# Performance work log

Measured on AMD Instinct MI355X. Metric: run time of the kernel, lower is better.

The kernel has to match this reference:

```python
import jax, jax.numpy as jnp
import numpy as np

B, D, H, C = 8192, 2048, 4096, 64
HALF = D // 2
BLOCKS = 2


def setup_inputs() -> dict:
    key = jax.random.key(0)
    ks = jax.random.split(key, 8)
    z = jax.random.normal(ks[0], (B, D), jnp.float32)
    condition = jax.random.normal(ks[1], (B, C), jnp.float32)
    # alternating masks: block 0 identity=odd indices, transform=even; block 1 flipped
    even = jnp.arange(0, D, 2, dtype=jnp.int32)
    odd = jnp.arange(1, D, 2, dtype=jnp.int32)
    idx_id = jnp.stack([odd, even])   # [BLOCKS, HALF]
    idx_tr = jnp.stack([even, odd])   # [BLOCKS, HALF]
    def init_w(k, shape, fan_in):
        return jax.random.normal(k, shape, jnp.float32) * np.float32(1.0 / np.sqrt(fan_in))
    W1 = init_w(ks[2], (BLOCKS, HALF + C, H), HALF + C)
    b1 = jnp.zeros((BLOCKS, H), jnp.float32)
    W2 = init_w(ks[3], (BLOCKS, H, H), H)
    b2 = jnp.zeros((BLOCKS, H), jnp.float32)
    W3 = init_w(ks[4], (BLOCKS, H, 2 * HALF), H) * np.float32(0.01)  # keep exp(S) tame
    b3 = jnp.zeros((BLOCKS, 2 * HALF), jnp.float32)
    return {"z": z, "condition": condition, "idx_id": idx_id, "idx_tr": idx_tr,
            "W1": W1, "b1": b1, "W2": W2, "b2": b2, "W3": W3, "b3": b3}


def reference(z, condition, idx_id, idx_tr, W1, b1, W2, b2, W3, b3):
    # F_zx of the affine coupling layer (scale_tanh=False, clamp_scale=None)
    x = z
    log_det = jnp.zeros((z.shape[0], 1), z.dtype)
    for i in range(BLOCKS):
        # gather identity channels, condition on external vector
        h = jnp.concatenate([x[:, idx_id[i]], condition], axis=-1)  # [B, HALF+C]
        h = jax.nn.relu(h @ W1[i] + b1[i])
        h = jax.nn.relu(h @ W2[i] + b2[i])
        out = (h @ W3[i] + b3[i]).reshape(x.shape[0], HALF, 2)
        S = out[..., 0]  # scale logits
        T = out[..., 1]  # translation
        # scatter-update transformed channels
        x = x.at[:, idx_tr[i]].set(x[:, idx_tr[i]] * jnp.exp(S) + T)
        log_det = log_det + jnp.sum(S, axis=1, keepdims=True)
    return x, log_det
```

## Files before the change

### kernel.cpp

```cpp
#include <hip/hip_runtime.h>
#include <hip/hip_bf16.h>

#define B_    8192
#define D_    2048
#define H_    4096
#define C_    64
#define HALF_ 1024
#define KIN_  1088

typedef __attribute__((ext_vector_type(8))) short bf16x8;
typedef __attribute__((ext_vector_type(4))) float f32x4;

__device__ __forceinline__ unsigned short f2bf(float f) {
  __hip_bfloat16 h = __float2bfloat16(f);
  return *reinterpret_cast<unsigned short*>(&h);
}

__device__ __forceinline__ void gload16(const void* g, void* s) {
  __builtin_amdgcn_global_load_lds((const __attribute__((address_space(1))) void*)g,
                                   (__attribute__((address_space(3))) void*)s,
                                   16, 0, 0);
}

__global__ void convT(const float* __restrict__ W, unsigned short* __restrict__ Wt,
                      int K, int N) {
  __shared__ float tile[32][33];
  int tx = threadIdx.x & 31, ty = threadIdx.x >> 5;
  int n0 = blockIdx.x * 32, k0 = blockIdx.y * 32;
#pragma unroll
  for (int i = 0; i < 4; ++i)
    tile[ty + i * 8][tx] = W[(size_t)(k0 + ty + i * 8) * N + n0 + tx];
  __syncthreads();
#pragma unroll
  for (int i = 0; i < 4; ++i)
    Wt[(size_t)(n0 + ty + i * 8) * K + k0 + tx] = f2bf(tile[tx][ty + i * 8]);
}

__global__ void build_act(const float* __restrict__ xsrc, const float* __restrict__ cond,
                          int par, unsigned short* __restrict__ A0) {
  int row = blockIdx.y;
  int col = blockIdx.x * 256 + threadIdx.x;
  if (col >= KIN_) return;
  float v = (col < HALF_) ? xsrc[(size_t)row * D_ + col * 2 + par]
                          : cond[(size_t)row * C_ + (col - HALF_)];
  A0[(size_t)row * KIN_ + col] = f2bf(v);
}

template <int MODE>
__global__ __launch_bounds__(512, 2)
void gemm8p(const unsigned short* __restrict__ A,
            const unsigned short* __restrict__ Bt,
            const float* __restrict__ bias,
            unsigned short* __restrict__ Cout,
            const float* __restrict__ xold, float* __restrict__ xnew,
            float* __restrict__ part, int par,
            int M, int N, int K) {
  __shared__ unsigned short lds[65536];
  char* ldsb = (char*)lds;
  const int tid = threadIdx.x;
  const int w = tid >> 6, lane = tid & 63;
  const int fr = lane & 15, fq = lane >> 4;
  const int wr = w >> 2, wc = w & 3;

  const int nbx = N >> 8;
  const int nwg = (int)gridDim.x;
  const int cpx = nwg >> 3;
  const int bid = (int)blockIdx.x;
  const int swz = (bid & 7) * cpx + (bid >> 3);
  const int by = swz / nbx, bx = swz - by * nbx;
  const int m0 = by << 8, n0 = bx << 8;

  const int chunkp = (((fr & 1) << 2) | fq) ^ (fr >> 1);
  const int A0 = (wr * 64 + (fr >> 1)) * 128 + chunkp * 16;
  const int B0 = 32768 + (wc * 32 + (fr >> 1)) * 128 + chunkp * 16;

  int rS[2], kcolS[2];
#pragma unroll
  for (int s = 0; s < 2; ++s) {
    int q = s * 512 + w * 64 + lane;
    int p = q >> 3, cph = q & 7;
    int clg = cph ^ (p & 7);
    rS[s] = 2 * p + (clg >> 2);
    kcolS[s] = (clg & 3) * 8;
  }
  const unsigned short* sA0 = A + (size_t)(m0 + rS[0]) * K + kcolS[0];
  const unsigned short* sA1 = A + (size_t)(m0 + rS[1]) * K + kcolS[1];
  const unsigned short* sB0 = Bt + (size_t)(n0 + rS[0]) * K + kcolS[0];
  const unsigned short* sB1 = Bt + (size_t)(n0 + rS[1]) * K + kcolS[1];
  const int dst0 = w * 1024 + lane * 16;

#define STAGE_A(KK, TILE, BUF) do {                                          \
    gload16(sA0 + (TILE) * 64 + (KK) * 32,                                   \
            ldsb + (BUF) + (KK) * 16384 + dst0);                             \
    gload16(sA1 + (TILE) * 64 + (KK) * 32,                                   \
            ldsb + (BUF) + (KK) * 16384 + 8192 + dst0);                      \
  } while (0)
#define STAGE_B(KK, TILE, BUF) do {                                          \
    gload16(sB0 + (TILE) * 64 + (KK) * 32,                                   \
            ldsb + (BUF) + 32768 + (KK) * 16384 + dst0);                     \
    gload16(sB1 + (TILE) * 64 + (KK) * 32,                                   \
            ldsb + (BUF) + 32768 + (KK) * 16384 + 8192 + dst0);              \
  } while (0)

  f32x4 acc[8][4];
  f32x4 z4 = {0.f, 0.f, 0.f, 0.f};
#pragma unroll
  for (int m = 0; m < 8; ++m)
#pragma unroll
    for (int n = 0; n < 4; ++n) acc[m][n] = z4;

  const int NT = K >> 6;

  STAGE_A(0, 0, 0);
  STAGE_A(1, 0, 0);
  STAGE_B(0, 0, 0);
  STAGE_B(1, 0, 0);
  STAGE_B(0, 1, 65536);
  STAGE_A(0, 1, 65536);
  STAGE_B(1, 1, 65536);
  asm volatile("s_waitcnt vmcnt(6)" ::: "memory");
  __builtin_amdgcn_sched_barrier(0);
  __builtin_amdgcn_s_barrier();

#define PHASE_TAIL()                                                         \
    __builtin_amdgcn_sched_barrier(0);                                       \
    __builtin_amdgcn_s_barrier();                                            \
    asm volatile("s_waitcnt lgkmcnt(0)" ::: "memory");                       \
    __builtin_amdgcn_sched_barrier(0);

#define TILE8(TT, S1, S234, DO_VM)                                           \
  {                                                                          \
    const int bufC = ((TT) & 1) * 65536;                                     \
    const int bufN = 65536 - bufC;                                           \
    bf16x8 av[4], bv[4];                                                     \
                               \
    _Pragma("unroll") for (int m = 0; m < 4; ++m)                            \
      av[m] = *(const bf16x8*)(ldsb + bufC + A0 + m * 1024);                 \
    _Pragma("unroll") for (int n = 0; n < 4; ++n)                            \
      bv[n] = *(const bf16x8*)(ldsb + bufC + B0 + n * 1024);                 \
    if (S1) { STAGE_A(1, (TT) + 1, bufN); }                                  \
    PHASE_TAIL()                                                             \
    __builtin_amdgcn_s_setprio(1);                                           \
    _Pragma("unroll") for (int m = 0; m < 4; ++m)                            \
      _Pragma("unroll") for (int n = 0; n < 4; ++n)                          \
        acc[m][n] = __builtin_amdgcn_mfma_f32_16x16x32_bf16(av[m], bv[n],    \
                                                        acc[m][n], 0, 0, 0); \
    __builtin_amdgcn_s_setprio(0);                                           \
    __builtin_amdgcn_sched_barrier(0);                                       \
    __builtin_amdgcn_s_barrier();                                            \
                                 \
    _Pragma("unroll") for (int m = 0; m < 4; ++m)                            \
      av[m] = *(const bf16x8*)(ldsb + bufC + A0 + (m + 4) * 1024);           \
    if (S234) { STAGE_B(0, (TT) + 2, bufC); }                                \
    PHASE_TAIL()                                                             \
    __builtin_amdgcn_s_setprio(1);                                           \
    _Pragma("unroll") for (int m = 0; m < 4; ++m)                            \
      _Pragma("unroll") for (int n = 0; n < 4; ++n)                          \
        acc[m + 4][n] = __builtin_amdgcn_mfma_f32_16x16x32_bf16(av[m], bv[n],\
                                                    acc[m + 4][n], 0, 0, 0); \
    __builtin_amdgcn_s_setprio(0);                                           \
    __builtin_amdgcn_sched_barrier(0);                                       \
    __builtin_amdgcn_s_barrier();                                            \
                               \
    _Pragma("unroll") for (int m = 0; m < 4; ++m)                            \
      av[m] = *(const bf16x8*)(ldsb + bufC + A0 + m * 1024 + 16384);         \
    _Pragma("unroll") for (int n = 0; n < 4; ++n)                            \
      bv[n] = *(const bf16x8*)(ldsb + bufC + B0 + n * 1024 + 16384);         \
    if (S234) { STAGE_A(0, (TT) + 2, bufC); }                                \
    PHASE_TAIL()                                                             \
    __builtin_amdgcn_s_setprio(1);                                           \
    _Pragma("unroll") for (int m = 0; m < 4; ++m)                            \
      _Pragma("unroll") for (int n = 0; n < 4; ++n)                          \
        acc[m][n] = __builtin_amdgcn_mfma_f32_16x16x32_bf16(av[m], bv[n],    \
                                                        acc[m][n], 0, 0, 0); \
    __builtin_amdgcn_s_setprio(0);                                           \
    __builtin_amdgcn_sched_barrier(0);                                       \
    __builtin_amdgcn_s_barrier();                                            \
                                           \
    _Pragma("unroll") for (int m = 0; m < 4; ++m)                            \
      av[m] = *(const bf16x8*)(ldsb + bufC + A0 + (m + 4) * 1024 + 16384);   \
    if (S234) { STAGE_B(1, (TT) + 2, bufC); }                                \
    PHASE_TAIL()                                                             \
    __builtin_amdgcn_s_setprio(1);                                           \
    _Pragma("unroll") for (int m = 0; m < 4; ++m)                            \
      _Pragma("unroll") for (int n = 0; n < 4; ++n)                          \
        acc[m + 4][n] = __builtin_amdgcn_mfma_f32_16x16x32_bf16(av[m], bv[n],\
                                                    acc[m + 4][n], 0, 0, 0); \
    __builtin_amdgcn_s_setprio(0);                                           \
    __builtin_amdgcn_sched_barrier(0);                                       \
    if (DO_VM == 1) asm volatile("s_waitcnt vmcnt(6)" ::: "memory");         \
    if (DO_VM == 2) asm volatile("s_waitcnt vmcnt(0)" ::: "memory");         \
    __builtin_amdgcn_sched_barrier(0);                                       \
    __builtin_amdgcn_s_barrier();                                            \
  }

  for (int T = 0; T < NT - 2; ++T) {
    TILE8(T, 1, 1, 1)
  }
  TILE8(NT - 2, 1, 0, 2)
  TILE8(NT - 1, 0, 0, 0)
#undef TILE8
#undef PHASE_TAIL
#undef STAGE_A
#undef STAGE_B

  if (MODE == 0) {
#pragma unroll
    for (int m = 0; m < 8; ++m)
#pragma unroll
      for (int n = 0; n < 4; ++n) {
        int gcol = n0 + wc * 64 + n * 16 + fr;
        float bb = bias[gcol];
#pragma unroll
        for (int r = 0; r < 4; ++r) {
          float v = fmaxf(acc[m][n][r] + bb, 0.f);
          int lrow = m * 16 + fq * 4 + r;
          *(unsigned short*)(ldsb + w * 16384 + lrow * 128 + ((n ^ fq) * 32) + fr * 2) = f2bf(v);
        }
      }
    asm volatile("s_waitcnt lgkmcnt(0)" ::: "memory");
    __builtin_amdgcn_sched_barrier(0);
    unsigned short* Cb = Cout + (size_t)(m0 + wr * 128) * N + n0 + wc * 64;
    const int sub = lane & 7;
#pragma unroll
    for (int i = 0; i < 16; ++i) {
      int lrow = i * 8 + (lane >> 3);
      int phys = (sub >> 1) ^ ((lrow >> 2) & 3);
      bf16x8 val = *(const bf16x8*)(ldsb + w * 16384 + lrow * 128 + phys * 32 + (sub & 1) * 16);
      *(bf16x8*)(Cb + (size_t)lrow * N + sub * 8) = val;
    }
  } else {
#pragma unroll
    for (int m = 0; m < 8; ++m) {
      float srow[4] = {0.f, 0.f, 0.f, 0.f};
#pragma unroll
      for (int n = 0; n < 4; ++n) {
        int gcol = n0 + wc * 64 + n * 16 + fr;
        float bb = bias[gcol];
#pragma unroll
        for (int r = 0; r < 4; ++r) {
          float v = acc[m][n][r] + bb;
          float vp = __shfl_xor(v, 1);
          if (!(fr & 1)) {
            int grow = m0 + wr * 128 + m * 16 + fq * 4 + r;
            float xo = xold[(size_t)grow * N + gcol + par];
            xnew[(size_t)grow * N + gcol + par] = xo * expf(v) + vp;
            srow[r] += v;
          }
        }
      }
#pragma unroll
      for (int r = 0; r < 4; ++r) {
        float s = srow[r];
        s += __shfl_xor(s, 2);
        s += __shfl_xor(s, 4);
        s += __shfl_xor(s, 8);
        if (fr == 0) {
          int grow = m0 + wr * 128 + m * 16 + fq * 4 + r;
          part[(size_t)grow * 32 + bx * 4 + wc] = s;
        }
      }
    }
  }
}

__global__ void reduce_logdet(const float* __restrict__ P, float* __restrict__ logdet, int add) {
  int row = blockIdx.x * 256 + threadIdx.x;
  float s = 0.f;
#pragma unroll
  for (int g = 0; g < 32; ++g) s += P[(size_t)row * 32 + g];
  logdet[row] = add ? (logdet[row] + s) : s;
}

extern "C" void kernel_launch(void* const* d_in, const int* in_sizes, int n_in,
                              void* d_out, int out_size, void* d_ws, size_t ws_size,
                              hipStream_t stream) {
  const float* z    = (const float*)d_in[0];
  const float* cond = (const float*)d_in[1];
  const float* W1   = (const float*)d_in[4];
  const float* b1   = (const float*)d_in[5];
  const float* W2   = (const float*)d_in[6];
  const float* b2   = (const float*)d_in[7];
  const float* W3   = (const float*)d_in[8];
  const float* b3   = (const float*)d_in[9];

  float* xout   = (float*)d_out;
  float* logdet = xout + (size_t)B_ * D_;

  char* ws = (char*)d_ws;
  unsigned short* Wt = (unsigned short*)ws;
  unsigned short* H1 = (unsigned short*)(ws + 33554432);
  unsigned short* H2 = (unsigned short*)(ws + 33554432 + 67108864);
  float* Pp = (float*)H1;
  unsigned short* A0 = H2;

  for (int blk = 0; blk < 2; ++blk) {
    const float* W1b = W1 + (size_t)blk * KIN_ * H_;
    const float* W2b = W2 + (size_t)blk * H_ * H_;
    const float* W3b = W3 + (size_t)blk * H_ * D_;
    const float* b1b = b1 + (size_t)blk * H_;
    const float* b2b = b2 + (size_t)blk * H_;
    const float* b3b = b3 + (size_t)blk * D_;
    const float* xsrc = blk ? xout : z;

    convT<<<dim3(H_ / 32, KIN_ / 32), 256, 0, stream>>>(W1b, Wt, KIN_, H_);
    build_act<<<dim3(5, B_), 256, 0, stream>>>(xsrc, cond, 1 - blk, A0);
    gemm8p<0><<<dim3((H_ / 256) * (B_ / 256)), 512, 0, stream>>>(
        A0, Wt, b1b, H1, nullptr, nullptr, nullptr, 0, B_, H_, KIN_);

    convT<<<dim3(H_ / 32, H_ / 32), 256, 0, stream>>>(W2b, Wt, H_, H_);
    gemm8p<0><<<dim3((H_ / 256) * (B_ / 256)), 512, 0, stream>>>(
        H1, Wt, b2b, H2, nullptr, nullptr, nullptr, 0, B_, H_, H_);

    convT<<<dim3(D_ / 32, H_ / 32), 256, 0, stream>>>(W3b, Wt, H_, D_);
    gemm8p<1><<<dim3((D_ / 256) * (B_ / 256)), 512, 0, stream>>>(
        H2, Wt, b3b, nullptr, z, xout, Pp, blk, B_, D_, H_);

    reduce_logdet<<<dim3(B_ / 256), 256, 0, stream>>>(Pp, logdet, blk);
  }
}
```

Baseline: 1.050 ms.

## Switch GEMM inner loop to 32x32x16 bf16 MFMA with new LDS fragment layout

Replaces the 16x16x32 MFMA tiles with 32x32x16 MFMA instructions. This reworks the per-lane LDS read offsets, the accumulator layout (4x2 f32x16) and both epilogues (the bf16 store and the affine-coupling/logdet reduction). The larger MFMA shape is meant to raise math density per LDS fragment read and cut instruction-issue overhead. It also vectorises the gather in build_act with float2 loads. The swizzle in the epilogue LDS staging was dropped, which risks LDS bank conflicts, and the new fragment mapping must match the 32x32 operand layout to stay correct.

```diff
diff --git a/kernel.cpp b/kernel.cpp
--- a/kernel.cpp
+++ b/kernel.cpp
@@ -10,6 +10,7 @@
 
 typedef __attribute__((ext_vector_type(8))) short bf16x8;
 typedef __attribute__((ext_vector_type(4))) float f32x4;
+typedef __attribute__((ext_vector_type(16))) float f32x16;
 
 __device__ __forceinline__ unsigned short f2bf(float f) {
   __hip_bfloat16 h = __float2bfloat16(f);
@@ -41,8 +42,13 @@
   int row = blockIdx.y;
   int col = blockIdx.x * 256 + threadIdx.x;
   if (col >= KIN_) return;
-  float v = (col < HALF_) ? xsrc[(size_t)row * D_ + col * 2 + par]
-                          : cond[(size_t)row * C_ + (col - HALF_)];
+  float v;
+  if (col < HALF_) {
+    float2 p = ((const float2*)xsrc)[(size_t)row * (D_ / 2) + col];
+    v = par ? p.y : p.x;
+  } else {
+    v = cond[(size_t)row * C_ + (col - HALF_)];
+  }
   A0[(size_t)row * KIN_ + col] = f2bf(v);
 }
 
@@ -59,7 +65,7 @@
   char* ldsb = (char*)lds;
   const int tid = threadIdx.x;
   const int w = tid >> 6, lane = tid & 63;
-  const int fr = lane & 15, fq = lane >> 4;
+  const int l31 = lane & 31, hi = lane >> 5;
   const int wr = w >> 2, wc = w & 3;
 
   const int nbx = N >> 8;
@@ -70,9 +76,20 @@
   const int by = swz / nbx, bx = swz - by * nbx;
   const int m0 = by << 8, n0 = bx << 8;
 
-  const int chunkp = (((fr & 1) << 2) | fq) ^ (fr >> 1);
-  const int A0 = (wr * 64 + (fr >> 1)) * 128 + chunkp * 16;
-  const int B0 = 32768 + (wc * 32 + (fr >> 1)) * 128 + chunkp * 16;
+  const int pline = l31 >> 1;
+  const int cb = ((lane & 1) << 2) | hi;
+  const int chunkE = (cb ^ (pline & 7)) * 16;
+  const int chunkO = ((cb | 2) ^ (pline & 7)) * 16;
+  const int Abase = (wr * 64 + pline) * 128;
+  const int Bbase = 32768 + (wc * 32 + pline) * 128;
+  int aoffs[4], boffs[4];
+#pragma unroll
+  for (int kk = 0; kk < 4; ++kk) {
+    int slab = (kk >> 1) * 16384;
+    int ch = (kk & 1) ? chunkO : chunkE;
+    aoffs[kk] = slab + Abase + ch;
+    boffs[kk] = slab + Bbase + ch;
+  }
 
   int rS[2], kcolS[2];
 #pragma unroll
@@ -102,12 +119,13 @@
             ldsb + (BUF) + 32768 + (KK) * 16384 + 8192 + dst0);              \
   } while (0)
 
-  f32x4 acc[8][4];
-  f32x4 z4 = {0.f, 0.f, 0.f, 0.f};
-#pragma unroll
-  for (int m = 0; m < 8; ++m)
-#pragma unroll
-    for (int n = 0; n < 4; ++n) acc[m][n] = z4;
+  f32x16 acc[4][2];
+#pragma unroll
+  for (int m = 0; m < 4; ++m)
+#pragma unroll
+    for (int n = 0; n < 2; ++n)
+#pragma unroll
+      for (int r = 0; r < 16; ++r) acc[m][n][r] = 0.f;
 
   const int NT = K >> 6;
 
@@ -128,64 +146,64 @@
     asm volatile("s_waitcnt lgkmcnt(0)" ::: "memory");                       \
     __builtin_amdgcn_sched_barrier(0);
 
-#define TILE8(TT, S1, S234, DO_VM)                                           \
+#define MFMA8(MB)                                                            \
+    __builtin_amdgcn_s_setprio(1);                                           \
+    _Pragma("unroll") for (int kk = 0; kk < 2; ++kk)                         \
+      _Pragma("unroll") for (int mm = 0; mm < 2; ++mm)                       \
+        _Pragma("unroll") for (int nn = 0; nn < 2; ++nn)                     \
+          acc[(MB) + mm][nn] = __builtin_amdgcn_mfma_f32_32x32x16_bf16(      \
+              av[mm][kk], bv[nn][kk], acc[(MB) + mm][nn], 0, 0, 0);          \
+    __builtin_amdgcn_s_setprio(0);                                           \
+    __builtin_amdgcn_sched_barrier(0);                                       \
+    __builtin_amdgcn_s_barrier();
+
+#define TILE32(TT, S1, S234, DO_VM)                                          \
   {                                                                          \
     const int bufC = ((TT) & 1) * 65536;                                     \
     const int bufN = 65536 - bufC;                                           \
-    bf16x8 av[4], bv[4];                                                     \
-                               \
-    _Pragma("unroll") for (int m = 0; m < 4; ++m)                            \
-      av[m] = *(const bf16x8*)(ldsb + bufC + A0 + m * 1024);                 \
-    _Pragma("unroll") for (int n = 0; n < 4; ++n)                            \
-      bv[n] = *(const bf16x8*)(ldsb + bufC + B0 + n * 1024);                 \
+    bf16x8 av[2][2], bv[2][2];                                               \
+                       \
+    _Pragma("unroll") for (int mm = 0; mm < 2; ++mm)                         \
+      _Pragma("unroll") for (int kk = 0; kk < 2; ++kk)                       \
+        av[mm][kk] = *(const bf16x8*)(ldsb + bufC + aoffs[kk] + mm * 2048);  \
+    _Pragma("unroll") for (int nn = 0; nn < 2; ++nn)                         \
+      _Pragma("unroll") for (int kk = 0; kk < 2; ++kk)                       \
+        bv[nn][kk] = *(const bf16x8*)(ldsb + bufC + boffs[kk] + nn * 2048);  \
     if (S1) { STAGE_A(1, (TT) + 1, bufN); }                                  \
     PHASE_TAIL()                                                             \
-    __builtin_amdgcn_s_setprio(1);                                           \
-    _Pragma("unroll") for (int m = 0; m < 4; ++m)                            \
-      _Pragma("unroll") for (int n = 0; n < 4; ++n)                          \
-        acc[m][n] = __builtin_amdgcn_mfma_f32_16x16x32_bf16(av[m], bv[n],    \
-                                                        acc[m][n], 0, 0, 0); \
-    __builtin_amdgcn_s_setprio(0);                                           \
-    __builtin_amdgcn_sched_barrier(0);                                       \
-    __builtin_amdgcn_s_barrier();                                            \
-                                 \
-    _Pragma("unroll") for (int m = 0; m < 4; ++m)                            \
-      av[m] = *(const bf16x8*)(ldsb + bufC + A0 + (m + 4) * 1024);           \
+    MFMA8(0)                                                                 \
+                            \
+    _Pragma("unroll") for (int mm = 0; mm < 2; ++mm)                         \
+      _Pragma("unroll") for (int kk = 0; kk < 2; ++kk)                       \
+        av[mm][kk] = *(const bf16x8*)(ldsb + bufC + aoffs[kk] + (mm + 2) * 2048); \
     if (S234) { STAGE_B(0, (TT) + 2, bufC); }                                \
     PHASE_TAIL()                                                             \
-    __builtin_amdgcn_s_setprio(1);                                           \
-    _Pragma("unroll") for (int m = 0; m < 4; ++m)                            \
-      _Pragma("unroll") for (int n = 0; n < 4; ++n)                          \
-        acc[m + 4][n] = __builtin_amdgcn_mfma_f32_16x16x32_bf16(av[m], bv[n],\
-                                                    acc[m + 4][n], 0, 0, 0); \
-    __builtin_amdgcn_s_setprio(0);                                           \
-    __builtin_amdgcn_sched_barrier(0);                                       \
-    __builtin_amdgcn_s_barrier();                                            \
-                               \
-    _Pragma("unroll") for (int m = 0; m < 4; ++m)                            \
-      av[m] = *(const bf16x8*)(ldsb + bufC + A0 + m * 1024 + 16384);         \
-    _Pragma("unroll") for (int n = 0; n < 4; ++n)                            \
-      bv[n] = *(const bf16x8*)(ldsb + bufC + B0 + n * 1024 + 16384);         \
+    MFMA8(2)                                                                 \
+                       \
+    _Pragma("unroll") for (int mm = 0; mm < 2; ++mm)                         \
+      _Pragma("unroll") for (int kk = 0; kk < 2; ++kk)                       \
+        av[mm][kk] = *(const bf16x8*)(ldsb + bufC + aoffs[kk + 2] + mm * 2048); \
+    _Pragma("unroll") for (int nn = 0; nn < 2; ++nn)                         \
+      _Pragma("unroll") for (int kk = 0; kk < 2; ++kk)                       \
+        bv[nn][kk] = *(const bf16x8*)(ldsb + bufC + boffs[kk + 2] + nn * 2048); \
     if (S234) { STAGE_A(0, (TT) + 2, bufC); }                                \
     PHASE_TAIL()                                                             \
+    MFMA8(0)                                                                 \
+                                       \
+    _Pragma("unroll") for (int mm = 0; mm < 2; ++mm)                         \
+      _Pragma("unroll") for (int kk = 0; kk < 2; ++kk)                       \
+        av[mm][kk] = *(const bf16x8*)(ldsb + bufC + aoffs[kk + 2] + (mm + 2) * 2048); \
+    if (S234) { STAGE_B(1, (TT) + 2, bufC); }                                \
+    __builtin_amdgcn_sched_barrier(0);                                       \
+    __builtin_amdgcn_s_barrier();                                            \
+    asm volatile("s_waitcnt lgkmcnt(0)" ::: "memory");                       \
+    __builtin_amdgcn_sched_barrier(0);                                       \
     __builtin_amdgcn_s_setprio(1);                                           \
-    _Pragma("unroll") for (int m = 0; m < 4; ++m)                            \
-      _Pragma("unroll") for (int n = 0; n < 4; ++n)                          \
-        acc[m][n] = __builtin_amdgcn_mfma_f32_16x16x32_bf16(av[m], bv[n],    \
-                                                        acc[m][n], 0, 0, 0); \
-    __builtin_amdgcn_s_setprio(0);                                           \
-    __builtin_amdgcn_sched_barrier(0);                                       \
-    __builtin_amdgcn_s_barrier();                                            \
-                                           \
-    _Pragma("unroll") for (int m = 0; m < 4; ++m)                            \
-      av[m] = *(const bf16x8*)(ldsb + bufC + A0 + (m + 4) * 1024 + 16384);   \
-    if (S234) { STAGE_B(1, (TT) + 2, bufC); }                                \
-    PHASE_TAIL()                                                             \
-    __builtin_amdgcn_s_setprio(1);                                           \
-    _Pragma("unroll") for (int m = 0; m < 4; ++m)                            \
-      _Pragma("unroll") for (int n = 0; n < 4; ++n)                          \
-        acc[m + 4][n] = __builtin_amdgcn_mfma_f32_16x16x32_bf16(av[m], bv[n],\
-                                                    acc[m + 4][n], 0, 0, 0); \
+    _Pragma("unroll") for (int kk = 0; kk < 2; ++kk)                         \
+      _Pragma("unroll") for (int mm = 0; mm < 2; ++mm)                       \
+        _Pragma("unroll") for (int nn = 0; nn < 2; ++nn)                     \
+          acc[mm + 2][nn] = __builtin_amdgcn_mfma_f32_32x32x16_bf16(         \
+              av[mm][kk], bv[nn][kk], acc[mm + 2][nn], 0, 0, 0);             \
     __builtin_amdgcn_s_setprio(0);                                           \
     __builtin_amdgcn_sched_barrier(0);                                       \
     if (DO_VM == 1) asm volatile("s_waitcnt vmcnt(6)" ::: "memory");         \
@@ -195,68 +213,69 @@
   }
 
   for (int T = 0; T < NT - 2; ++T) {
-    TILE8(T, 1, 1, 1)
-  }
-  TILE8(NT - 2, 1, 0, 2)
-  TILE8(NT - 1, 0, 0, 0)
-#undef TILE8
+    TILE32(T, 1, 1, 1)
+  }
+  TILE32(NT - 2, 1, 0, 2)
+  TILE32(NT - 1, 0, 0, 0)
+#undef TILE32
+#undef MFMA8
 #undef PHASE_TAIL
 #undef STAGE_A
 #undef STAGE_B
 
   if (MODE == 0) {
 #pragma unroll
-    for (int m = 0; m < 8; ++m)
-#pragma unroll
-      for (int n = 0; n < 4; ++n) {
-        int gcol = n0 + wc * 64 + n * 16 + fr;
-        float bb = bias[gcol];
-#pragma unroll
-        for (int r = 0; r < 4; ++r) {
+    for (int n = 0; n < 2; ++n) {
+      float bb = bias[n0 + wc * 64 + n * 32 + l31];
+#pragma unroll
+      for (int m = 0; m < 4; ++m)
+#pragma unroll
+        for (int r = 0; r < 16; ++r) {
           float v = fmaxf(acc[m][n][r] + bb, 0.f);
-          int lrow = m * 16 + fq * 4 + r;
-          *(unsigned short*)(ldsb + w * 16384 + lrow * 128 + ((n ^ fq) * 32) + fr * 2) = f2bf(v);
+          int lrow = m * 32 + (r & 3) + 8 * (r >> 2) + 4 * hi;
+          *(unsigned short*)(ldsb + w * 16384 + lrow * 128 + (n * 32 + l31) * 2) = f2bf(v);
         }
-      }
+    }
     asm volatile("s_waitcnt lgkmcnt(0)" ::: "memory");
     __builtin_amdgcn_sched_barrier(0);
     unsigned short* Cb = Cout + (size_t)(m0 + wr * 128) * N + n0 + wc * 64;
-    const int sub = lane & 7;
 #pragma unroll
     for (int i = 0; i < 16; ++i) {
       int lrow = i * 8 + (lane >> 3);
-      int phys = (sub >> 1) ^ ((lrow >> 2) & 3);
-      bf16x8 val = *(const bf16x8*)(ldsb + w * 16384 + lrow * 128 + phys * 32 + (sub & 1) * 16);
-      *(bf16x8*)(Cb + (size_t)lrow * N + sub * 8) = val;
+      bf16x8 val = *(const bf16x8*)(ldsb + w * 16384 + lrow * 128 + (lane & 7) * 16);
+      *(bf16x8*)(Cb + (size_t)lrow * N + (lane & 7) * 8) = val;
     }
   } else {
 #pragma unroll
-    for (int m = 0; m < 8; ++m) {
-      float srow[4] = {0.f, 0.f, 0.f, 0.f};
-#pragma unroll
-      for (int n = 0; n < 4; ++n) {
-        int gcol = n0 + wc * 64 + n * 16 + fr;
+    for (int m = 0; m < 4; ++m) {
+      float sr[16];
+#pragma unroll
+      for (int r = 0; r < 16; ++r) sr[r] = 0.f;
+#pragma unroll
+      for (int n = 0; n < 2; ++n) {
+        int gcol = n0 + wc * 64 + n * 32 + l31;
         float bb = bias[gcol];
 #pragma unroll
-        for (int r = 0; r < 4; ++r) {
+        for (int r = 0; r < 16; ++r) {
           float v = acc[m][n][r] + bb;
           float vp = __shfl_xor(v, 1);
-          if (!(fr & 1)) {
-            int grow = m0 + wr * 128 + m * 16 + fq * 4 + r;
-            float xo = xold[(size_t)grow * N + gcol + par];
-            xnew[(size_t)grow * N + gcol + par] = xo * expf(v) + vp;
-            srow[r] += v;
+          if (!(lane & 1)) {
+            int grow = m0 + wr * 128 + m * 32 + (r & 3) + 8 * (r >> 2) + 4 * hi;
+            size_t idx = (size_t)grow * N + gcol + par;
+            xnew[idx] = xold[idx] * expf(v) + vp;
+            sr[r] += v;
           }
         }
       }
 #pragma unroll
-      for (int r = 0; r < 4; ++r) {
-        float s = srow[r];
+      for (int r = 0; r < 16; ++r) {
+        float s = sr[r];
         s += __shfl_xor(s, 2);
         s += __shfl_xor(s, 4);
         s += __shfl_xor(s, 8);
-        if (fr == 0) {
-          int grow = m0 + wr * 128 + m * 16 + fq * 4 + r;
+        s += __shfl_xor(s, 16);
+        if (l31 == 0) {
+          int grow = m0 + wr * 128 + m * 32 + (r & 3) + 8 * (r >> 2) + 4 * hi;
           part[(size_t)grow * 32 + bx * 4 + wc] = s;
         }
       }
```

Result: slower. 1.169 ms (+11.3%).
